# Kernel tuning notes

Measured on AMD Instinct MI355X. Metric: run time of the kernel, lower is better.

Reference implementation:

```python
import jax, jax.numpy as jnp
import numpy as np

N_EMBD = 1024
BLOCK_SIZE = 2048
ATTN_SPAN = 256
LN_EPS = 1e-5


def _band_mask(T, span, dtype):
    ones = jnp.ones((T, T), dtype=dtype)
    # tril(.,0) * (1 - tril(.,-span)) -> causal band of width `span`
    return jnp.tril(ones, 0) * (1.0 - jnp.tril(ones, -span))


def setup_inputs() -> dict:
    key = jax.random.key(0)
    k_x, k_w, k_b, k_lw = jax.random.split(key, 4)
    B, T, C = 4, BLOCK_SIZE, N_EMBD
    x = jax.random.normal(k_x, (B, T, C), dtype=jnp.float32)
    # qkv_net: Linear(C, 3C) with bias (torch default)
    lim = 1.0 / np.sqrt(C)
    W_qkv = jax.random.uniform(k_w, (C, 3 * C), minval=-lim, maxval=lim, dtype=jnp.float32)
    b_qkv = jax.random.uniform(k_b, (3 * C,), minval=-lim, maxval=lim, dtype=jnp.float32)
    ln_w = jnp.ones((C,), dtype=jnp.float32)
    ln_b = jnp.zeros((C,), dtype=jnp.float32)
    return {"x": x, "W_qkv": W_qkv, "b_qkv": b_qkv, "ln_w": ln_w, "ln_b": ln_b}


def _layer_norm(h, w, b):
    mu = jnp.mean(h, axis=-1, keepdims=True)
    var = jnp.var(h, axis=-1, keepdims=True)
    return (h - mu) * jax.lax.rsqrt(var + LN_EPS) * w + b


def reference(x, W_qkv, b_qkv, ln_w, ln_b):
    B, T, C = x.shape
    qkv = x @ W_qkv + b_qkv  # [B,T,3C]
    q, k, v = jnp.split(qkv, 3, axis=-1)
    scale = np.sqrt(C * ATTN_SPAN).astype(np.float32)
    scores = jnp.einsum('bid,bjd->bij', q, k) / scale  # [B,T,T]
    scores = scores * _band_mask(T, ATTN_SPAN, x.dtype)[None, :, :]
    out = jnp.einsum('bij,bjd->bid', scores, v)  # [B,T,C]
    return _layer_norm(out, ln_w, ln_b)
```

## Files before the change

kernel.cpp:

```cpp
#include <hip/hip_runtime.h>
#include <cstdint>
#include <cstddef>

#define N_EMBD 1024
#define T_SEQ  2048
#define NBATCH 4
#define SPAN   256
#define C3     3072

typedef float  floatx4 __attribute__((ext_vector_type(4)));
typedef __bf16 bf16x8  __attribute__((ext_vector_type(8)));

__device__ inline unsigned short f2bf(float f) {
    union { float f; unsigned u; } x; x.f = f;
    unsigned u = x.u;
    unsigned r = (u + 0x7fffu + ((u >> 16) & 1u)) >> 16;
    return (unsigned short)r;
}

typedef __attribute__((address_space(1))) const void GVOID;
typedef __attribute__((address_space(3))) void LVOID;
__device__ inline void gl2lds16(const void* g, void* l) {
    __builtin_amdgcn_global_load_lds((GVOID*)g, (LVOID*)l, 16, 0, 0);
}

__device__ inline void stage128x32(const unsigned short* g, size_t stride,
                                   unsigned short* lds, int lane, int wave) {
    const int r     = wave * 16 + (lane >> 2);
    const int chunk = (lane & 3) ^ ((r >> 1) & 3);
    const unsigned short* src = g + (size_t)r * stride + chunk * 8;
    gl2lds16(src,               &lds[(wave * 16) * 32]);
    gl2lds16(src + 64 * stride, &lds[(64 + wave * 16) * 32]);
}

__device__ inline void stage64x64(const unsigned short* g, size_t stride,
                                  unsigned short* lds, int lane, int wave) {
#pragma unroll
    for (int rnd = 0; rnd < 2; rnd++) {
        const int r = rnd * 32 + wave * 8 + (lane >> 3);
        const int chunk = (lane & 7) ^ (r & 7);
        gl2lds16(g + (size_t)r * stride + chunk * 8, &lds[(rnd * 32 + wave * 8) * 64]);
    }
}

__device__ inline void stage128x64(const unsigned short* g, size_t stride,
                                   unsigned short* lds, int lane, int wave) {
#pragma unroll
    for (int rnd = 0; rnd < 4; rnd++) {
        const int r = rnd * 32 + wave * 8 + (lane >> 3);
        const int chunk = (lane & 7) ^ (r & 7);
        gl2lds16(g + (size_t)r * stride + chunk * 8, &lds[(rnd * 32 + wave * 8) * 64]);
    }
}

__global__ __launch_bounds__(256) void k_prep(const float* __restrict__ x,
                                              unsigned short* __restrict__ Xb,
                                              const float* __restrict__ W,
                                              unsigned short* __restrict__ WbT) {
    __shared__ unsigned short t[32][33];
    if (blockIdx.x < 8192) {
        int i = (blockIdx.x * 256 + threadIdx.x) * 4;
        float4 v = *(const float4*)(x + i);
        ushort4 o;
        o.x = f2bf(v.x); o.y = f2bf(v.y); o.z = f2bf(v.z); o.w = f2bf(v.w);
        *(ushort4*)(Xb + i) = o;
    } else {
        int bid = blockIdx.x - 8192;
        int k0 = (bid & 31) * 32, n0 = (bid >> 5) * 32;
        int tx = threadIdx.x & 31, ty = threadIdx.x >> 5;
#pragma unroll
        for (int i = 0; i < 4; i++) {
            int k = k0 + ty + i * 8;
            t[ty + i * 8][tx] = f2bf(W[(size_t)k * C3 + n0 + tx]);
        }
        __syncthreads();
#pragma unroll
        for (int i = 0; i < 4; i++) {
            int n = n0 + ty + i * 8;
            WbT[(size_t)n * N_EMBD + k0 + tx] = t[tx][ty + i * 8];
        }
    }
}

__global__ __launch_bounds__(256) void k_gemm(const unsigned short* __restrict__ Xb,
                                              const unsigned short* __restrict__ WbT,
                                              const float* __restrict__ bqkv,
                                              unsigned short* __restrict__ QK,
                                              unsigned short* __restrict__ Vt) {
    __shared__ unsigned short As[4096];
    __shared__ unsigned short Bs[4096];
    const int tid = threadIdx.x, lane = tid & 63, wave = tid >> 6;
    const int bx = blockIdx.x, m0 = blockIdx.y * 128;
    const bool isV = (bx >= 16);
    const int n0 = isV ? (2048 + (bx - 16) * 128) : (bx * 128);
    const int wr = wave >> 1, wc = wave & 1;

    floatx4 acc[4][4] = {};

    const unsigned short* gA = (isV ? WbT + (size_t)n0 * N_EMBD : Xb  + (size_t)m0 * N_EMBD);
    const unsigned short* gB = (isV ? Xb  + (size_t)m0 * N_EMBD : WbT + (size_t)n0 * N_EMBD);
    const int qk = ((lane >> 4) ^ ((lane >> 1) & 3)) * 8;
    const int ra = wr * 64 + (lane & 15);
    const int rb = wc * 64 + (lane & 15);

    for (int k0 = 0; k0 < N_EMBD; k0 += 32) {
        stage128x32(gA + k0, N_EMBD, As, lane, wave);
        stage128x32(gB + k0, N_EMBD, Bs, lane, wave);
        __syncthreads();
        bf16x8 a[4], b[4];
#pragma unroll
        for (int mi = 0; mi < 4; mi++) a[mi] = *(const bf16x8*)&As[(ra + mi * 16) * 32 + qk];
#pragma unroll
        for (int ni = 0; ni < 4; ni++) b[ni] = *(const bf16x8*)&Bs[(rb + ni * 16) * 32 + qk];
#pragma unroll
        for (int mi = 0; mi < 4; mi++)
#pragma unroll
            for (int ni = 0; ni < 4; ni++)
                acc[mi][ni] = __builtin_amdgcn_mfma_f32_16x16x32_bf16(a[mi], b[ni], acc[mi][ni], 0, 0, 0);
        __syncthreads();
    }

    const int cn = lane & 15, q = lane >> 4;
    if (!isV) {
#pragma unroll
        for (int ni = 0; ni < 4; ni++) {
            const int n = n0 + wc * 64 + ni * 16 + cn;
            const float bias = bqkv[n];
#pragma unroll
            for (int mi = 0; mi < 4; mi++) {
                const int mbase = m0 + wr * 64 + mi * 16 + q * 4;
#pragma unroll
                for (int r = 0; r < 4; r++)
                    QK[(size_t)(mbase + r) * 2048 + n] = f2bf(acc[mi][ni][r] + bias);
            }
        }
    } else {
        const int bb = m0 >> 11, tg0 = (m0 & 2047);
        const int cb = n0 - 2048;
#pragma unroll
        for (int mi = 0; mi < 4; mi++) {
            const int cbase = wr * 64 + mi * 16 + q * 4;
#pragma unroll
            for (int r = 0; r < 4; r++) {
                const int c = cbase + r;
                const float bias = bqkv[n0 + c];
                unsigned short* dst = Vt + ((size_t)(bb * 1024 + cb + c)) * 2048 + tg0;
#pragma unroll
                for (int ni = 0; ni < 4; ni++)
                    dst[wc * 64 + ni * 16 + cn] = f2bf(acc[mi][ni][r] + bias);
            }
        }
    }
}

__global__ __launch_bounds__(256) void k_scores(const unsigned short* __restrict__ QK,
                                                unsigned short* __restrict__ S) {
    const int jj = blockIdx.x, qb = blockIdx.y, b = blockIdx.z;
    const int jb = qb - 4 + jj;
    if (jb < 0) return;

    __shared__ unsigned short Qs[4096];
    __shared__ unsigned short Ks[4096];
    const int tid = threadIdx.x, lane = tid & 63, wave = tid >> 6;
    const int wr = wave >> 1, wc = wave & 1;
    const int n15 = lane & 15, q = lane >> 4;

    floatx4 acc[2][2] = {};

    const unsigned short* gQ = QK + ((size_t)(b * T_SEQ + qb * 64)) * 2048;
    const unsigned short* gK = QK + ((size_t)(b * T_SEQ + jb * 64)) * 2048 + 1024;

    for (int k0 = 0; k0 < N_EMBD; k0 += 64) {
        stage64x64(gQ + k0, 2048, Qs, lane, wave);
        stage64x64(gK + k0, 2048, Ks, lane, wave);
        __syncthreads();
#pragma unroll
        for (int s = 0; s < 2; s++) {
            bf16x8 a[2], bbf[2];
#pragma unroll
            for (int mi = 0; mi < 2; mi++) {
                const int row = wr * 32 + mi * 16 + n15;
                a[mi] = *(const bf16x8*)&Qs[row * 64 + (((s * 4 + q) ^ (row & 7)) * 8)];
            }
#pragma unroll
            for (int ni = 0; ni < 2; ni++) {
                const int row = wc * 32 + ni * 16 + n15;
                bbf[ni] = *(const bf16x8*)&Ks[row * 64 + (((s * 4 + q) ^ (row & 7)) * 8)];
            }
#pragma unroll
            for (int mi = 0; mi < 2; mi++)
#pragma unroll
                for (int ni = 0; ni < 2; ni++)
                    acc[mi][ni] = __builtin_amdgcn_mfma_f32_16x16x32_bf16(a[mi], bbf[ni], acc[mi][ni], 0, 0, 0);
        }
        __syncthreads();
    }

    unsigned short* Sb = S + (((size_t)(b * 32 + qb) * 5 + jj) << 12);
#pragma unroll
    for (int mi = 0; mi < 2; mi++)
#pragma unroll
        for (int ni = 0; ni < 2; ni++)
#pragma unroll
            for (int r = 0; r < 4; r++) {
                const int il = wr * 32 + mi * 16 + q * 4 + r;
                const int jl = wc * 32 + ni * 16 + n15;
                const int gi = qb * 64 + il, gj = jb * 64 + jl;
                const float v = ((gj <= gi) && (gj > gi - SPAN)) ? acc[mi][ni][r] * (1.0f / 512.0f) : 0.0f;
                Sb[il * 64 + jl] = f2bf(v);
            }
}

__global__ __launch_bounds__(256) void k_sv(const unsigned short* __restrict__ S,
                                            const unsigned short* __restrict__ Vt,
                                            float* __restrict__ out) {
    const int cg = blockIdx.x, qb = blockIdx.y, b = blockIdx.z;
    const int c0 = cg * 128;

    __shared__ unsigned short Ss[4096];
    __shared__ unsigned short Vs[8192];
    const int tid = threadIdx.x, lane = tid & 63, wave = tid >> 6;
    const int wr = wave >> 1, wc = wave & 1;
    const int n15 = lane & 15, q = lane >> 4;

    floatx4 acc[2][4] = {};

    for (int jj = 0; jj < 5; jj++) {
        const int jb = qb - 4 + jj;
        if (jb < 0) continue;
        stage64x64(S + (((size_t)(b * 32 + qb) * 5 + jj) << 12), 64, Ss, lane, wave);
        stage128x64(Vt + ((size_t)(b * 1024 + c0)) * 2048 + jb * 64, 2048, Vs, lane, wave);
        __syncthreads();
#pragma unroll
        for (int s = 0; s < 2; s++) {
            bf16x8 a[2], bbf[4];
#pragma unroll
            for (int mi = 0; mi < 2; mi++) {
                const int row = wr * 32 + mi * 16 + n15;
                a[mi] = *(const bf16x8*)&Ss[row * 64 + (((s * 4 + q) ^ (row & 7)) * 8)];
            }
#pragma unroll
            for (int ni = 0; ni < 4; ni++) {
                const int row = wc * 64 + ni * 16 + n15;
                bbf[ni] = *(const bf16x8*)&Vs[row * 64 + (((s * 4 + q) ^ (row & 7)) * 8)];
            }
#pragma unroll
            for (int mi = 0; mi < 2; mi++)
#pragma unroll
                for (int ni = 0; ni < 4; ni++)
                    acc[mi][ni] = __builtin_amdgcn_mfma_f32_16x16x32_bf16(a[mi], bbf[ni], acc[mi][ni], 0, 0, 0);
        }
        __syncthreads();
    }

#pragma unroll
    for (int mi = 0; mi < 2; mi++)
#pragma unroll
        for (int ni = 0; ni < 4; ni++)
#pragma unroll
            for (int r = 0; r < 4; r++) {
                const int il = wr * 32 + mi * 16 + q * 4 + r;
                const int cl = wc * 64 + ni * 16 + n15;
                out[((size_t)(b * T_SEQ + qb * 64 + il)) * N_EMBD + c0 + cl] = acc[mi][ni][r];
            }
}

__global__ __launch_bounds__(256) void k_ln(float* __restrict__ out,
                                            const float* __restrict__ w,
                                            const float* __restrict__ bias) {
    __shared__ float red[8];
    const int t = threadIdx.x;
    float* p = out + (size_t)blockIdx.x * N_EMBD;
    float4 v = ((const float4*)p)[t];
    float s  = v.x + v.y + v.z + v.w;
    float sq = v.x * v.x + v.y * v.y + v.z * v.z + v.w * v.w;
#pragma unroll
    for (int off = 32; off; off >>= 1) {
        s  += __shfl_down(s, off, 64);
        sq += __shfl_down(sq, off, 64);
    }
    const int wave = t >> 6, lane = t & 63;
    if (lane == 0) { red[wave] = s; red[4 + wave] = sq; }
    __syncthreads();
    const float ts = red[0] + red[1] + red[2] + red[3];
    const float tq = red[4] + red[5] + red[6] + red[7];
    const float mean = ts * (1.0f / N_EMBD);
    const float var  = tq * (1.0f / N_EMBD) - mean * mean;
    const float rs = rsqrtf(var + 1e-5f);
    float4 wv = ((const float4*)w)[t];
    float4 bv = ((const float4*)bias)[t];
    float4 o;
    o.x = (v.x - mean) * rs * wv.x + bv.x;
    o.y = (v.y - mean) * rs * wv.y + bv.y;
    o.z = (v.z - mean) * rs * wv.z + bv.z;
    o.w = (v.w - mean) * rs * wv.w + bv.w;
    ((float4*)p)[t] = o;
}

extern "C" void kernel_launch(void* const* d_in, const int* in_sizes, int n_in,
                              void* d_out, int out_size, void* d_ws, size_t ws_size,
                              hipStream_t stream) {
    const float* x  = (const float*)d_in[0];
    const float* W  = (const float*)d_in[1];
    const float* bq = (const float*)d_in[2];
    const float* lw = (const float*)d_in[3];
    const float* lb = (const float*)d_in[4];
    float* out = (float*)d_out;
    char* ws = (char*)d_ws;

    unsigned short* Xb   = (unsigned short*)(ws + 0);
    unsigned short* Sbuf = (unsigned short*)(ws + 0);
    unsigned short* WbT  = (unsigned short*)(ws + 16777216);
    unsigned short* QK   = (unsigned short*)(ws + 23068672);
    unsigned short* Vt   = (unsigned short*)(ws + 56623104);

    k_prep   <<<11264,           256, 0, stream>>>(x, Xb, W, WbT);
    k_gemm   <<<dim3(24, 64),    256, 0, stream>>>(Xb, WbT, bq, QK, Vt);
    k_scores <<<dim3(5, 32, 4),  256, 0, stream>>>(QK, Sbuf);
    k_sv     <<<dim3(8, 32, 4),  256, 0, stream>>>(Sbuf, Vt, out);
    k_ln     <<<8192,            256, 0, stream>>>(out, lw, lb);
}
```

Baseline: 214.4 us.

## Widen K-tiles in score and SV kernels and add occupancy hint to GEMM

The score kernel now stages 64x128 K-slices with a 16-way XOR swizzle, which halves the number of sync-separated iterations over the embedding dimension. The SV kernel loads two key blocks into separate LDS buffers per round, so three synchronised rounds replace five. The QKV GEMM gets a minimum-occupancy launch bound of 6 blocks. These changes cut barrier and load-latency stalls in exchange for more LDS per block, which may lower occupancy, and the GEMM hint may cause register spills.

```diff
diff --git a/kernel.cpp b/kernel.cpp
--- a/kernel.cpp
+++ b/kernel.cpp
@@ -50,6 +50,16 @@
         const int r = rnd * 32 + wave * 8 + (lane >> 3);
         const int chunk = (lane & 7) ^ (r & 7);
         gl2lds16(g + (size_t)r * stride + chunk * 8, &lds[(rnd * 32 + wave * 8) * 64]);
+    }
+}
+
+__device__ inline void stage64x128(const unsigned short* g, size_t stride,
+                                   unsigned short* lds, int lane, int wave) {
+#pragma unroll
+    for (int rnd = 0; rnd < 4; rnd++) {
+        const int r = rnd * 16 + wave * 4 + (lane >> 4);
+        const int chunk = (lane & 15) ^ (r & 15);
+        gl2lds16(g + (size_t)r * stride + chunk * 8, &lds[(rnd * 16 + wave * 4) * 128]);
     }
 }
 
@@ -82,11 +92,11 @@
     }
 }
 
-__global__ __launch_bounds__(256) void k_gemm(const unsigned short* __restrict__ Xb,
-                                              const unsigned short* __restrict__ WbT,
-                                              const float* __restrict__ bqkv,
-                                              unsigned short* __restrict__ QK,
-                                              unsigned short* __restrict__ Vt) {
+__global__ __launch_bounds__(256, 6) void k_gemm(const unsigned short* __restrict__ Xb,
+                                                 const unsigned short* __restrict__ WbT,
+                                                 const float* __restrict__ bqkv,
+                                                 unsigned short* __restrict__ QK,
+                                                 unsigned short* __restrict__ Vt) {
     __shared__ unsigned short As[4096];
     __shared__ unsigned short Bs[4096];
     const int tid = threadIdx.x, lane = tid & 63, wave = tid >> 6;
@@ -159,8 +169,8 @@
     const int jb = qb - 4 + jj;
     if (jb < 0) return;
 
-    __shared__ unsigned short Qs[4096];
-    __shared__ unsigned short Ks[4096];
+    __shared__ unsigned short Qs[8192];
+    __shared__ unsigned short Ks[8192];
     const int tid = threadIdx.x, lane = tid & 63, wave = tid >> 6;
     const int wr = wave >> 1, wc = wave & 1;
     const int n15 = lane & 15, q = lane >> 4;
@@ -170,22 +180,23 @@
     const unsigned short* gQ = QK + ((size_t)(b * T_SEQ + qb * 64)) * 2048;
     const unsigned short* gK = QK + ((size_t)(b * T_SEQ + jb * 64)) * 2048 + 1024;
 
-    for (int k0 = 0; k0 < N_EMBD; k0 += 64) {
-        stage64x64(gQ + k0, 2048, Qs, lane, wave);
-        stage64x64(gK + k0, 2048, Ks, lane, wave);
-        __syncthreads();
-#pragma unroll
-        for (int s = 0; s < 2; s++) {
+    for (int k0 = 0; k0 < N_EMBD; k0 += 128) {
+        stage64x128(gQ + k0, 2048, Qs, lane, wave);
+        stage64x128(gK + k0, 2048, Ks, lane, wave);
+        __syncthreads();
+#pragma unroll
+        for (int kb = 0; kb < 4; kb++) {
+            const int s = kb * 4 + q;
             bf16x8 a[2], bbf[2];
 #pragma unroll
             for (int mi = 0; mi < 2; mi++) {
                 const int row = wr * 32 + mi * 16 + n15;
-                a[mi] = *(const bf16x8*)&Qs[row * 64 + (((s * 4 + q) ^ (row & 7)) * 8)];
+                a[mi] = *(const bf16x8*)&Qs[row * 128 + ((s ^ (row & 15)) * 8)];
             }
 #pragma unroll
             for (int ni = 0; ni < 2; ni++) {
                 const int row = wc * 32 + ni * 16 + n15;
-                bbf[ni] = *(const bf16x8*)&Ks[row * 64 + (((s * 4 + q) ^ (row & 7)) * 8)];
+                bbf[ni] = *(const bf16x8*)&Ks[row * 128 + ((s ^ (row & 15)) * 8)];
             }
 #pragma unroll
             for (int mi = 0; mi < 2; mi++)
@@ -217,38 +228,50 @@
     const int cg = blockIdx.x, qb = blockIdx.y, b = blockIdx.z;
     const int c0 = cg * 128;
 
-    __shared__ unsigned short Ss[4096];
-    __shared__ unsigned short Vs[8192];
+    __shared__ unsigned short Ss[2][4096];
+    __shared__ unsigned short Vs[2][8192];
     const int tid = threadIdx.x, lane = tid & 63, wave = tid >> 6;
     const int wr = wave >> 1, wc = wave & 1;
     const int n15 = lane & 15, q = lane >> 4;
 
     floatx4 acc[2][4] = {};
 
-    for (int jj = 0; jj < 5; jj++) {
-        const int jb = qb - 4 + jj;
-        if (jb < 0) continue;
-        stage64x64(S + (((size_t)(b * 32 + qb) * 5 + jj) << 12), 64, Ss, lane, wave);
-        stage128x64(Vt + ((size_t)(b * 1024 + c0)) * 2048 + jb * 64, 2048, Vs, lane, wave);
-        __syncthreads();
-#pragma unroll
-        for (int s = 0; s < 2; s++) {
-            bf16x8 a[2], bbf[4];
-#pragma unroll
-            for (int mi = 0; mi < 2; mi++) {
-                const int row = wr * 32 + mi * 16 + n15;
-                a[mi] = *(const bf16x8*)&Ss[row * 64 + (((s * 4 + q) ^ (row & 7)) * 8)];
-            }
-#pragma unroll
-            for (int ni = 0; ni < 4; ni++) {
-                const int row = wc * 64 + ni * 16 + n15;
-                bbf[ni] = *(const bf16x8*)&Vs[row * 64 + (((s * 4 + q) ^ (row & 7)) * 8)];
-            }
-#pragma unroll
-            for (int mi = 0; mi < 2; mi++)
-#pragma unroll
-                for (int ni = 0; ni < 4; ni++)
-                    acc[mi][ni] = __builtin_amdgcn_mfma_f32_16x16x32_bf16(a[mi], bbf[ni], acc[mi][ni], 0, 0, 0);
+    for (int jr = 0; jr < 3; jr++) {
+#pragma unroll
+        for (int p = 0; p < 2; p++) {
+            const int jj = jr * 2 + p;
+            if (jj >= 5) break;
+            const int jb = qb - 4 + jj;
+            if (jb < 0) continue;
+            stage64x64(S + (((size_t)(b * 32 + qb) * 5 + jj) << 12), 64, Ss[p], lane, wave);
+            stage128x64(Vt + ((size_t)(b * 1024 + c0)) * 2048 + jb * 64, 2048, Vs[p], lane, wave);
+        }
+        __syncthreads();
+#pragma unroll
+        for (int p = 0; p < 2; p++) {
+            const int jj = jr * 2 + p;
+            if (jj >= 5) break;
+            const int jb = qb - 4 + jj;
+            if (jb < 0) continue;
+#pragma unroll
+            for (int s = 0; s < 2; s++) {
+                bf16x8 a[2], bbf[4];
+#pragma unroll
+                for (int mi = 0; mi < 2; mi++) {
+                    const int row = wr * 32 + mi * 16 + n15;
+                    a[mi] = *(const bf16x8*)&Ss[p][row * 64 + (((s * 4 + q) ^ (row & 7)) * 8)];
+                }
+#pragma unroll
+                for (int ni = 0; ni < 4; ni++) {
+                    const int row = wc * 64 + ni * 16 + n15;
+                    bbf[ni] = *(const bf16x8*)&Vs[p][row * 64 + (((s * 4 + q) ^ (row & 7)) * 8)];
+                }
+#pragma unroll
+                for (int mi = 0; mi < 2; mi++)
+#pragma unroll
+                    for (int ni = 0; ni < 4; ni++)
+                        acc[mi][ni] = __builtin_amdgcn_mfma_f32_16x16x32_bf16(a[mi], bbf[ni], acc[mi][ni], 0, 0, 0);
+            }
         }
         __syncthreads();
     }
```

After: 489.1 us. 2.28x slower.
